# Performance work log

Hardware: AMD Instinct MI355X
Metric: run time of the kernel (lower is better)

The kernel has to match this reference:

```python
import jax, jax.numpy as jnp
import numpy as np

N = 100_000        # nodes
E = 800_000        # directed edges before symmetrization
IN_DIM = 18        # input_dim_wf + input_dim_vm
HID = 128
VM_NUM = 16        # each_vm_type_num * vm_types
B = 65536 // VM_NUM
NEG_SLOPE = 0.2    # PyG GATConv leaky_relu slope


def _gat_conv(h, src, dst, W, a_s, a_d, b, n):
    """PyG GATConv (heads=1, add_self_loops=True, dropout off)."""
    z = h @ W                                     # [n, C]
    loops = jnp.arange(n, dtype=src.dtype)
    s = jnp.concatenate([src, loops])
    d = jnp.concatenate([dst, loops])
    e_s = z @ a_s                                 # [n]
    e_d = z @ a_d
    alpha = jax.nn.leaky_relu(e_s[s] + e_d[d], NEG_SLOPE)   # [E']
    amax = jax.ops.segment_max(alpha, d, num_segments=n)    # stable softmax over incoming edges
    ex = jnp.exp(alpha - amax[d])
    denom = jax.ops.segment_sum(ex, d, num_segments=n)
    w = ex / denom[d]
    out = jax.ops.segment_sum(w[:, None] * z[s], d, num_segments=n)
    return out + b


def setup_inputs() -> dict:
    key = jax.random.key(0)
    ks = jax.random.split(key, 16)
    sc = 0.1
    inp = {
        'state_wf': jax.random.normal(ks[0], (N, IN_DIM), jnp.float32),
        'edge_index': jax.random.randint(ks[1], (2, E), 0, N, jnp.int32),
        'candidate_task_index': jax.random.randint(ks[2], (B * VM_NUM,), 0, N, jnp.int32),
        # GAT layer 0: 18 -> 128
        'W0': jax.random.normal(ks[3], (IN_DIM, HID), jnp.float32) * sc,
        'a_src0': jax.random.normal(ks[4], (HID,), jnp.float32) * sc,
        'a_dst0': jax.random.normal(ks[5], (HID,), jnp.float32) * sc,
        'b0': jnp.zeros((HID,), jnp.float32),
        # GAT layer 1: 128 -> 128
        'W1': jax.random.normal(ks[6], (HID, HID), jnp.float32) * sc,
        'a_src1': jax.random.normal(ks[7], (HID,), jnp.float32) * sc,
        'a_dst1': jax.random.normal(ks[8], (HID,), jnp.float32) * sc,
        'b1': jnp.zeros((HID,), jnp.float32),
        # actor MLP: Linear(128,128) + ReLU + Linear(128,1)
        'mW0': jax.random.normal(ks[9], (HID, HID), jnp.float32) * sc,
        'mb0': jnp.zeros((HID,), jnp.float32),
        'mW1': jax.random.normal(ks[10], (HID, 1), jnp.float32) * sc,
        'mb1': jnp.zeros((1,), jnp.float32),
    }
    return inp


def reference(state_wf, edge_index, candidate_task_index,
              W0, a_src0, a_dst0, b0, W1, a_src1, a_dst1, b1,
              mW0, mb0, mW1, mb1):
    # Actor.forward symmetrizes edges: cat(edge_index, edge_index.flip(0))
    src = jnp.concatenate([edge_index[0], edge_index[1]])
    dst = jnp.concatenate([edge_index[1], edge_index[0]])
    # GAT stack, F.elu after each conv (dropout=0)
    h = jax.nn.elu(_gat_conv(state_wf, src, dst, W0, a_src0, a_dst0, b0, N))
    h = jax.nn.elu(_gat_conv(h, src, dst, W1, a_src1, a_dst1, b1, N))
    # gather candidate tasks and score them
    cand = h[candidate_task_index].reshape(-1, VM_NUM, HID)       # [B, vm, H]
    scores = jax.nn.relu(cand @ mW0 + mb0) @ mW1 + mb1            # [B, vm, 1]
    pi = jax.nn.softmax(scores, axis=1)[..., 0]                   # softmax over dim=1
    return pi
```

## Files before the change

kernel.cpp:

```cpp
#include <hip/hip_runtime.h>
#include <hip/hip_bf16.h>
#include <math.h>
#include <stdint.h>

typedef __hip_bfloat16 bf16;
typedef __attribute__((ext_vector_type(8))) short s8v;
typedef __attribute__((ext_vector_type(4))) float f4v;

#define N_NODES 100000
#define HID 128
#define NEG 0.2f
#define NBUCK 256
#define BSHIFT 9
#define INDIM 18
#define CAP 10240

__device__ __forceinline__ float b2f(bf16 x) { return __bfloat162float(x); }
__device__ __forceinline__ bf16 f2b(float x) { return __float2bfloat16(x); }
__device__ __forceinline__ float lo_bf(unsigned int u) {
    union { unsigned int i; float f; } c; c.i = u << 16; return c.f;
}
__device__ __forceinline__ float hi_bf(unsigned int u) {
    union { unsigned int i; float f; } c; c.i = u & 0xffff0000u; return c.f;
}
__device__ __forceinline__ short bfbits(float x) {
    union { bf16 b; short s; } u; u.b = f2b(x); return u.s;
}


__device__ void pack128(const float* __restrict__ W, short* __restrict__ frag, int b) {
    int idx = b * 256 + threadIdx.x;
    int j = idx & 7;
    int lane = (idx >> 3) & 63;
    int cb = (idx >> 9) & 7;
    int kb = idx >> 12;
    int k = kb * 32 + (lane >> 4) * 8 + j;
    int c = cb * 16 + (lane & 15);
    float w = W[k * HID + c];
    bf16 hi = f2b(w);
    frag[idx] = bfbits(w);
    frag[16384 + idx] = bfbits(w - b2f(hi));
}

__global__ __launch_bounds__(256) void k_prep(const float* __restrict__ W1,
                          const float* __restrict__ mW0, const float* __restrict__ W0,
                          short* __restrict__ W1f, short* __restrict__ mW0f,
                          short* __restrict__ W0f, int* __restrict__ bnext) {
    int b = blockIdx.x;
    int t = threadIdx.x;
    if (b < 64) { pack128(W1, W1f, b); return; }
    if (b < 128) { pack128(mW0, mW0f, b - 64); return; }
    if (b < 192) {
        int idx = (b - 128) * 256 + t;
        int var = idx >> 13;
        int r = idx & 8191;
        int j = r & 7;
        int lane = (r >> 3) & 63;
        int cb = (r >> 9) & 7;
        int kb = r >> 12;
        int kp = kb * 32 + (lane >> 4) * 8 + j;
        int c = cb * 16 + (lane & 15);
        short out = 0;
        if (kp < 2 * INDIM) {
            int src = (kp < INDIM) ? kp : kp - INDIM;
            float w = W0[src * HID + c];
            bf16 hi = f2b(w);
            bool want_hi = (kp < INDIM) ^ (var == 1);
            out = want_hi ? bfbits(w) : bfbits(w - b2f(hi));
        }
        W0f[var * 8192 + r] = out;
        return;
    }
    bnext[t] = t * CAP;
}


#define SCH 2048
#define SK 8
__global__ __launch_bounds__(256) void k_scat_feat0(const int* __restrict__ ei, int E,
                        int* __restrict__ bnext, unsigned* __restrict__ pairs, int nscat,
                        const float* __restrict__ x, const short* __restrict__ Wf,
                        const float* __restrict__ as_, const float* __restrict__ ad_,
                        bf16* __restrict__ z, float* __restrict__ es, float* __restrict__ ed,
                        int n) {
    __shared__ int h[NBUCK], base[NBUCK], h2[NBUCK];
    __shared__ __align__(16) short ztile[4][16][136];
    if (blockIdx.x < (unsigned)nscat) {
        int t = threadIdx.x;
        h[t] = 0; h2[t] = 0;
        __syncthreads();
        int b0 = blockIdx.x * SCH;
        int eu[SK], ev[SK];
#pragma unroll
        for (int k = 0; k < SK; k++) {
            int i = b0 + k * 256 + t;
            if (i < E) {
                int u = ei[i], v = ei[E + i];
                eu[k] = u; ev[k] = v;
                atomicAdd(&h[v >> BSHIFT], 1);
                atomicAdd(&h[u >> BSHIFT], 1);
            } else { eu[k] = -1; ev[k] = -1; }
        }
        __syncthreads();
        if (h[t] > 0) base[t] = atomicAdd(&bnext[t], h[t]);
        __syncthreads();
#pragma unroll
        for (int k = 0; k < SK; k++) {
            if (eu[k] >= 0) {
                unsigned u = (unsigned)eu[k], v = (unsigned)ev[k];
                int bv = v >> BSHIFT;
                pairs[base[bv] + atomicAdd(&h2[bv], 1)] = ((v & 511u) << 17) | u;
                int bu = u >> BSHIFT;
                pairs[base[bu] + atomicAdd(&h2[bu], 1)] = ((u & 511u) << 17) | v;
            }
        }
        return;
    }
    int fb = blockIdx.x - nscat;
    int wv = threadIdx.x >> 6, lane = threadIdx.x & 63;
    int node0 = (fb * 4 + wv) * 16;
    if (node0 >= n) return;
    int m = lane & 15, q = lane >> 4;
    const float* xr = x + (size_t)(node0 + m) * INDIM;
    s8v af0, af1;
#pragma unroll
    for (int j = 0; j < 8; j++) {
        int p0 = q * 8 + j;
        float v0 = 0.f;
        if (p0 < INDIM) v0 = xr[p0];
        else if (p0 < 2 * INDIM) v0 = xr[p0 - INDIM];
        short o0;
        if (p0 < INDIM) o0 = bfbits(v0);
        else o0 = bfbits(v0 - b2f(f2b(v0)));
        af0[j] = o0;
        int p1 = 32 + q * 8 + j;
        float v1 = (p1 < 2 * INDIM) ? xr[p1 - INDIM] : 0.f;
        af1[j] = bfbits(v1 - b2f(f2b(v1)));
    }
    f4v acc[8];
#pragma unroll
    for (int cb = 0; cb < 8; cb++) acc[cb] = (f4v){0.f, 0.f, 0.f, 0.f};
    const s8v* wf = (const s8v*)Wf;
#pragma unroll
    for (int cb = 0; cb < 8; cb++) {
        acc[cb] = __builtin_amdgcn_mfma_f32_16x16x32_bf16(af0, wf[cb * 64 + lane], acc[cb], 0, 0, 0);
        acc[cb] = __builtin_amdgcn_mfma_f32_16x16x32_bf16(af1, wf[(8 + cb) * 64 + lane], acc[cb], 0, 0, 0);
        acc[cb] = __builtin_amdgcn_mfma_f32_16x16x32_bf16(af0, wf[1024 + cb * 64 + lane], acc[cb], 0, 0, 0);
        acc[cb] = __builtin_amdgcn_mfma_f32_16x16x32_bf16(af1, wf[1024 + (8 + cb) * 64 + lane], acc[cb], 0, 0, 0);
    }
    float pe[4] = {0.f, 0.f, 0.f, 0.f}, pd[4] = {0.f, 0.f, 0.f, 0.f};
#pragma unroll
    for (int cb = 0; cb < 8; cb++) {
        float asv = as_[cb * 16 + m];
        float adv = ad_[cb * 16 + m];
#pragma unroll
        for (int r = 0; r < 4; r++) { pe[r] += acc[cb][r] * asv; pd[r] += acc[cb][r] * adv; }
    }
#pragma unroll
    for (int r = 0; r < 4; r++) {
#pragma unroll
        for (int off = 1; off < 16; off <<= 1) {
            pe[r] += __shfl_xor(pe[r], off);
            pd[r] += __shfl_xor(pd[r], off);
        }
    }
    if (m == 0) {
#pragma unroll
        for (int r = 0; r < 4; r++) {
            es[node0 + q * 4 + r] = pe[r];
            ed[node0 + q * 4 + r] = pd[r];
        }
    }
#pragma unroll
    for (int cb = 0; cb < 8; cb++)
#pragma unroll
        for (int r = 0; r < 4; r++)
            ztile[wv][q * 4 + r][cb * 16 + m] = bfbits(acc[cb][r]);
#pragma unroll
    for (int i = 0; i < 4; i++) {
        int idx = i * 64 + lane;
        int row = idx >> 4, t = idx & 15;
        s8v v = *(const s8v*)&ztile[wv][row][t * 8];
        *(s8v*)((short*)z + (size_t)(node0 + row) * HID + t * 8) = v;
    }
}


__global__ __launch_bounds__(256) void k_bbuild(const unsigned* __restrict__ pairs,
                                                const int* __restrict__ bnext,
                                                int* __restrict__ rowptr,
                                                int* __restrict__ col, int n) {
    __shared__ int deg[512];
    __shared__ int off[512];
    __shared__ int s2[2][256];
    __shared__ int exs[256];
    int t = threadIdx.x;
    int b = blockIdx.x;
    int node0 = b << BSHIFT;
    int cnt = bnext[t] - t * CAP;
    s2[0][t] = cnt;
    __syncthreads();
    int cur = 0;
    for (int o = 1; o < 256; o <<= 1) {
        int x2 = s2[cur][t] + ((t >= o) ? s2[cur][t - o] : 0);
        s2[cur ^ 1][t] = x2;
        cur ^= 1;
        __syncthreads();
    }
    exs[t] = s2[cur][t] - cnt;
    __syncthreads();
    int out0 = exs[b];
    int in0 = b * CAP;
    int cnt_b = bnext[b] - in0;
    deg[t] = 0; deg[t + 256] = 0;
    __syncthreads();
    for (int i = t; i < cnt_b; i += 256) atomicAdd(&deg[pairs[in0 + i] >> 17], 1);
    __syncthreads();
    int a0 = deg[2 * t], a1 = deg[2 * t + 1];
    int s = a0 + a1;
    s2[0][t] = s;
    __syncthreads();
    cur = 0;
    for (int o = 1; o < 256; o <<= 1) {
        int x2 = s2[cur][t] + ((t >= o) ? s2[cur][t - o] : 0);
        s2[cur ^ 1][t] = x2;
        cur ^= 1;
        __syncthreads();
    }
    int excl = s2[cur][t] - s;
    off[2 * t] = excl;
    off[2 * t + 1] = excl + a0;
    __syncthreads();
    for (int j = t; j < 512; j += 256) {
        int node = node0 + j;
        if (node <= n) rowptr[node] = out0 + off[j];
    }
    deg[t] = 0; deg[t + 256] = 0;
    __syncthreads();
    for (int i = t; i < cnt_b; i += 256) {
        unsigned pr = pairs[in0 + i];
        int d = pr >> 17;
        int ofs = atomicAdd(&deg[d], 1);
        col[out0 + off[d] + ofs] = (int)(pr & 0x1FFFFu);
    }
}


__global__ __launch_bounds__(256) void k_aggfeat1(const bf16* __restrict__ z,
                      const int* __restrict__ rowptr, const int* __restrict__ col,
                      const float* __restrict__ es, const float* __restrict__ ed,
                      const float* __restrict__ bias,
                      const short* __restrict__ Wf, const float* __restrict__ as1,
                      const float* __restrict__ ad1,
                      bf16* __restrict__ zout, float* __restrict__ es1,
                      float* __restrict__ ed1, int n) {
    __shared__ __align__(16) short htile[16][136];
    __shared__ __align__(16) short ztile[16][136];
    __shared__ float red[4][16][2];
    int wv = threadIdx.x >> 6, lane = threadIdx.x & 63;
    int node0 = blockIdx.x * 16;
    int g = lane >> 4, t = lane & 15;
    const uint4* zr = (const uint4*)z;
    for (int i = 0; i < 4; i++) {
        int d = node0 + wv * 4 + i;
        int s0 = rowptr[d], s1 = rowptr[d + 1];
        float edv = ed[d];
        float acc[8];
#pragma unroll
        for (int j = 0; j < 8; j++) acc[j] = 0.f;
        float den = 0.f;
        for (int e0 = s0; e0 < s1; e0 += 8) {
            int eA = e0 + g, eB = e0 + 4 + g;
            bool okA = (eA < s1), okB = (eB < s1);
            int sA = col[okA ? eA : s1 - 1];
            int sB = col[okB ? eB : s1 - 1];
            float aA = es[sA] + edv; aA = aA > 0.f ? aA : NEG * aA;
            float aB = es[sB] + edv; aB = aB > 0.f ? aB : NEG * aB;
            float pA = okA ? __expf(fminf(aA, 15.f)) : 0.f;
            float pB = okB ? __expf(fminf(aB, 15.f)) : 0.f;
            uint4 rA = zr[(size_t)sA * 16 + t];
            uint4 rB = zr[(size_t)sB * 16 + t];
            den += pA + pB;
            acc[0] += pA * lo_bf(rA.x) + pB * lo_bf(rB.x);
            acc[1] += pA * hi_bf(rA.x) + pB * hi_bf(rB.x);
            acc[2] += pA * lo_bf(rA.y) + pB * lo_bf(rB.y);
            acc[3] += pA * hi_bf(rA.y) + pB * hi_bf(rB.y);
            acc[4] += pA * lo_bf(rA.z) + pB * lo_bf(rB.z);
            acc[5] += pA * hi_bf(rA.z) + pB * hi_bf(rB.z);
            acc[6] += pA * lo_bf(rA.w) + pB * lo_bf(rB.w);
            acc[7] += pA * hi_bf(rA.w) + pB * hi_bf(rB.w);
        }
#pragma unroll
        for (int off = 16; off <= 32; off <<= 1) {
            den += __shfl_xor(den, off);
#pragma unroll
            for (int j = 0; j < 8; j++) acc[j] += __shfl_xor(acc[j], off);
        }
        if (g == 0) {
            float aself = es[d] + edv;
            aself = aself > 0.f ? aself : NEG * aself;
            float pself = __expf(fminf(aself, 15.f));
            den += pself;
            uint4 raw = zr[(size_t)d * 16 + t];
            acc[0] += pself * lo_bf(raw.x); acc[1] += pself * hi_bf(raw.x);
            acc[2] += pself * lo_bf(raw.y); acc[3] += pself * hi_bf(raw.y);
            acc[4] += pself * lo_bf(raw.z); acc[5] += pself * hi_bf(raw.z);
            acc[6] += pself * lo_bf(raw.w); acc[7] += pself * hi_bf(raw.w);
            float inv = 1.f / den;
            union { bf16 hv[8]; uint4 v; } uo;
#pragma unroll
            for (int j = 0; j < 8; j++) {
                float o = acc[j] * inv + bias[t * 8 + j];
                o = o > 0.f ? o : (__expf(o) - 1.f);
                uo.hv[j] = f2b(o);
            }
            *((uint4*)&htile[wv * 4 + i][t * 8]) = uo.v;
        }
    }
    __syncthreads();
    int m = lane & 15, q = lane >> 4;
    s8v af[4];
#pragma unroll
    for (int kb = 0; kb < 4; kb++) af[kb] = *(const s8v*)&htile[m][kb * 32 + q * 8];
    f4v fac[2];
    fac[0] = (f4v){0.f, 0.f, 0.f, 0.f};
    fac[1] = (f4v){0.f, 0.f, 0.f, 0.f};
    const s8v* wf = (const s8v*)Wf;
#pragma unroll
    for (int kb = 0; kb < 4; kb++) {
#pragma unroll
        for (int c = 0; c < 2; c++) {
            int cb = 2 * wv + c;
            fac[c] = __builtin_amdgcn_mfma_f32_16x16x32_bf16(af[kb], wf[(kb * 8 + cb) * 64 + lane], fac[c], 0, 0, 0);
            fac[c] = __builtin_amdgcn_mfma_f32_16x16x32_bf16(af[kb], wf[2048 + (kb * 8 + cb) * 64 + lane], fac[c], 0, 0, 0);
        }
    }
    float pe[4] = {0.f, 0.f, 0.f, 0.f}, pd[4] = {0.f, 0.f, 0.f, 0.f};
#pragma unroll
    for (int c = 0; c < 2; c++) {
        int cb = 2 * wv + c;
        float asv = as1[cb * 16 + m];
        float adv = ad1[cb * 16 + m];
#pragma unroll
        for (int r = 0; r < 4; r++) { pe[r] += fac[c][r] * asv; pd[r] += fac[c][r] * adv; }
    }
#pragma unroll
    for (int r = 0; r < 4; r++) {
#pragma unroll
        for (int off = 1; off < 16; off <<= 1) {
            pe[r] += __shfl_xor(pe[r], off);
            pd[r] += __shfl_xor(pd[r], off);
        }
    }
    if (m == 0) {
#pragma unroll
        for (int r = 0; r < 4; r++) {
            red[wv][q * 4 + r][0] = pe[r];
            red[wv][q * 4 + r][1] = pd[r];
        }
    }
#pragma unroll
    for (int c = 0; c < 2; c++) {
        int cb = 2 * wv + c;
#pragma unroll
        for (int r = 0; r < 4; r++)
            ztile[q * 4 + r][cb * 16 + m] = bfbits(fac[c][r]);
    }
    __syncthreads();
    int tid = threadIdx.x;
    if (tid < 16) es1[node0 + tid] = red[0][tid][0] + red[1][tid][0] + red[2][tid][0] + red[3][tid][0];
    else if (tid < 32) {
        int c = tid - 16;
        ed1[node0 + c] = red[0][c][1] + red[1][c][1] + red[2][c][1] + red[3][c][1];
    }
    int row = tid >> 4, tt = tid & 15;
    s8v v = *(const s8v*)&ztile[row][tt * 8];
    *(s8v*)((short*)zout + (size_t)(node0 + row) * HID + tt * 8) = v;
}


__global__ __launch_bounds__(256) void k_agg(const bf16* __restrict__ z,
                      const int* __restrict__ rowptr, const int* __restrict__ col,
                      const float* __restrict__ es, const float* __restrict__ ed,
                      const float* __restrict__ bias, bf16* __restrict__ hout, int n) {
    int wv = threadIdx.x >> 6;
    int lane = threadIdx.x & 63;
    int d = blockIdx.x * 4 + wv;
    if (d >= n) return;
    int s0 = rowptr[d], s1 = rowptr[d + 1];
    float edv = ed[d];
    int g = lane >> 4, t = lane & 15;
    const uint4* zr = (const uint4*)z;
    float acc[8];
#pragma unroll
    for (int j = 0; j < 8; j++) acc[j] = 0.f;
    float den = 0.f;
    for (int e0 = s0; e0 < s1; e0 += 8) {
        int eA = e0 + g, eB = e0 + 4 + g;
        bool okA = (eA < s1), okB = (eB < s1);
        int sA = col[okA ? eA : s1 - 1];
        int sB = col[okB ? eB : s1 - 1];
        float aA = es[sA] + edv; aA = aA > 0.f ? aA : NEG * aA;
        float aB = es[sB] + edv; aB = aB > 0.f ? aB : NEG * aB;
        float pA = okA ? __expf(fminf(aA, 15.f)) : 0.f;
        float pB = okB ? __expf(fminf(aB, 15.f)) : 0.f;
        uint4 rA = zr[(size_t)sA * 16 + t];
        uint4 rB = zr[(size_t)sB * 16 + t];
        den += pA + pB;
        acc[0] += pA * lo_bf(rA.x) + pB * lo_bf(rB.x);
        acc[1] += pA * hi_bf(rA.x) + pB * hi_bf(rB.x);
        acc[2] += pA * lo_bf(rA.y) + pB * lo_bf(rB.y);
        acc[3] += pA * hi_bf(rA.y) + pB * hi_bf(rB.y);
        acc[4] += pA * lo_bf(rA.z) + pB * lo_bf(rB.z);
        acc[5] += pA * hi_bf(rA.z) + pB * hi_bf(rB.z);
        acc[6] += pA * lo_bf(rA.w) + pB * lo_bf(rB.w);
        acc[7] += pA * hi_bf(rA.w) + pB * hi_bf(rB.w);
    }
#pragma unroll
    for (int off = 16; off <= 32; off <<= 1) {
        den += __shfl_xor(den, off);
#pragma unroll
        for (int j = 0; j < 8; j++) acc[j] += __shfl_xor(acc[j], off);
    }
    if (g == 0) {
        float aself = es[d] + edv;
        aself = aself > 0.f ? aself : NEG * aself;
        float pself = __expf(fminf(aself, 15.f));
        den += pself;
        uint4 raw = zr[(size_t)d * 16 + t];
        acc[0] += pself * lo_bf(raw.x); acc[1] += pself * hi_bf(raw.x);
        acc[2] += pself * lo_bf(raw.y); acc[3] += pself * hi_bf(raw.y);
        acc[4] += pself * lo_bf(raw.z); acc[5] += pself * hi_bf(raw.z);
        acc[6] += pself * lo_bf(raw.w); acc[7] += pself * hi_bf(raw.w);
        float inv = 1.f / den;
        union { bf16 hv[8]; uint4 v; } uo;
#pragma unroll
        for (int j = 0; j < 8; j++) {
            float o = acc[j] * inv + bias[t * 8 + j];
            o = o > 0.f ? o : (__expf(o) - 1.f);
            uo.hv[j] = f2b(o);
        }
        ((uint4*)hout)[(size_t)d * 16 + t] = uo.v;
    }
}


__global__ __launch_bounds__(256) void k_group(const bf16* __restrict__ h,
                        const int* __restrict__ cand,
                        const short* __restrict__ Wf, const float* __restrict__ mb0,
                        const float* __restrict__ mW1, const float* __restrict__ mb1,
                        float* __restrict__ out) {
    __shared__ float sc[4][16];
    int wv = threadIdx.x >> 6, lane = threadIdx.x & 63;
    int g = blockIdx.x * 4 + wv;
    int m = lane & 15, q = lane >> 4;
    int node = cand[g * 16 + m];
    const short* hrow = (const short*)h + (size_t)node * HID + q * 8;
    s8v af[4];
#pragma unroll
    for (int kb = 0; kb < 4; kb++) af[kb] = *(const s8v*)(hrow + kb * 32);
    f4v acc[8];
#pragma unroll
    for (int cb = 0; cb < 8; cb++) acc[cb] = (f4v){0.f, 0.f, 0.f, 0.f};
    const s8v* wf = (const s8v*)Wf;
#pragma unroll
    for (int kb = 0; kb < 4; kb++) {
#pragma unroll
        for (int cb = 0; cb < 8; cb++) {
            acc[cb] = __builtin_amdgcn_mfma_f32_16x16x32_bf16(af[kb], wf[(kb * 8 + cb) * 64 + lane], acc[cb], 0, 0, 0);
            acc[cb] = __builtin_amdgcn_mfma_f32_16x16x32_bf16(af[kb], wf[2048 + (kb * 8 + cb) * 64 + lane], acc[cb], 0, 0, 0);
        }
    }
    float sr[4] = {0.f, 0.f, 0.f, 0.f};
#pragma unroll
    for (int cb = 0; cb < 8; cb++) {
        float b0v = mb0[cb * 16 + m];
        float w1v = mW1[cb * 16 + m];
#pragma unroll
        for (int r = 0; r < 4; r++) sr[r] += fmaxf(acc[cb][r] + b0v, 0.f) * w1v;
    }
#pragma unroll
    for (int r = 0; r < 4; r++) {
#pragma unroll
        for (int off = 1; off < 16; off <<= 1) sr[r] += __shfl_xor(sr[r], off);
    }
    float b1v = mb1[0];
    if (m == 0) {
#pragma unroll
        for (int r = 0; r < 4; r++) sc[wv][q * 4 + r] = sr[r] + b1v;
    }
    if (lane < 16) {
        float s = sc[wv][lane];
        float mx = s;
#pragma unroll
        for (int off = 1; off < 16; off <<= 1) mx = fmaxf(mx, __shfl_xor(mx, off));
        float e = __expf(s - mx);
        float den = e;
#pragma unroll
        for (int off = 1; off < 16; off <<= 1) den += __shfl_xor(den, off);
        out[g * 16 + lane] = e / den;
    }
}


extern "C" void kernel_launch(void* const* d_in, const int* in_sizes, int n_in,
                              void* d_out, int out_size, void* d_ws, size_t ws_size,
                              hipStream_t stream) {
    const int N = N_NODES;
    const float* state = (const float*)d_in[0];
    const int* ei   = (const int*)d_in[1];
    const int* cand = (const int*)d_in[2];
    const float* W0  = (const float*)d_in[3];
    const float* as0 = (const float*)d_in[4];
    const float* ad0 = (const float*)d_in[5];
    const float* b0  = (const float*)d_in[6];
    const float* W1  = (const float*)d_in[7];
    const float* as1 = (const float*)d_in[8];
    const float* ad1 = (const float*)d_in[9];
    const float* b1  = (const float*)d_in[10];
    const float* mW0 = (const float*)d_in[11];
    const float* mb0 = (const float*)d_in[12];
    const float* mW1 = (const float*)d_in[13];
    const float* mb1 = (const float*)d_in[14];

    int E = in_sizes[1] / 2;
    int M = 2 * E;
    int ncand = in_sizes[2];
    int ngroups = ncand / 16;

    char* p = (char*)d_ws;
    bf16* zb = (bf16*)p;              p += (size_t)N * HID * 2;
    bf16* hb = (bf16*)p;              p += (size_t)N * HID * 2;
    float* es = (float*)p;            p += (size_t)N * 4;
    float* ed = (float*)p;            p += (size_t)N * 4;
    float* es1 = (float*)p;           p += (size_t)N * 4;
    float* ed1 = (float*)p;           p += (size_t)N * 4;
    p = (char*)(((uintptr_t)p + 15) & ~(uintptr_t)15);
    short* W1frag  = (short*)p;       p += 32768 * 2;
    short* mW0frag = (short*)p;       p += 32768 * 2;
    short* W0frag  = (short*)p;       p += 16384 * 2;
    int* rowptr = (int*)p;            p += (size_t)(N + 1) * 4;
    int* col    = (int*)p;            p += (size_t)M * 4;
    unsigned* pairs = (unsigned*)p;   p += (size_t)NBUCK * CAP * 4;
    int* bnext  = (int*)p;            p += NBUCK * 4;

    int nwb = N / 4;
    int nfb = (N / 16 + 3) / 4;
    int nscat = (E + SCH - 1) / SCH;

    k_prep<<<193, 256, 0, stream>>>(W1, mW0, W0, W1frag, mW0frag, W0frag, bnext);
    k_scat_feat0<<<nscat + nfb, 256, 0, stream>>>(ei, E, bnext, pairs, nscat,
                                                  state, W0frag, as0, ad0, zb, es, ed, N);
    k_bbuild<<<NBUCK, 256, 0, stream>>>(pairs, bnext, rowptr, col, N);
    k_aggfeat1<<<N / 16, 256, 0, stream>>>(zb, rowptr, col, es, ed, b0,
                                           W1frag, as1, ad1, hb, es1, ed1, N);
    k_agg<<<nwb, 256, 0, stream>>>(hb, rowptr, col, es1, ed1, b1, zb, N);
    k_group<<<ngroups / 4, 256, 0, stream>>>(zb, cand, mW0frag, mb0, mW1, mb1, (float*)d_out);
}
```

Baseline: 310.7 us.

## Make each wave own 16 nodes in fused layer-1 aggregate+transform, drop block barriers

Restructures k_aggfeat1 so each wavefront aggregates 16 destination nodes and then computes the full 128-column projection for its own tile, instead of four waves sharing a 16-node tile and splitting the columns. This removes both __syncthreads barriers and the cross-wave shared-memory reduction of the attention logits, so waves with short neighbour lists no longer wait on slow ones. In exchange each wave holds 8 MFMA accumulators (more registers, possibly lower occupancy), loads the whole W1 fragment set per wave, and the grid has a quarter as many blocks.

```diff
diff --git a/kernel.cpp b/kernel.cpp
--- a/kernel.cpp
+++ b/kernel.cpp
@@ -254,15 +254,14 @@
                       const float* __restrict__ ad1,
                       bf16* __restrict__ zout, float* __restrict__ es1,
                       float* __restrict__ ed1, int n) {
-    __shared__ __align__(16) short htile[16][136];
-    __shared__ __align__(16) short ztile[16][136];
-    __shared__ float red[4][16][2];
+    __shared__ __align__(16) short htile[4][16][136];
     int wv = threadIdx.x >> 6, lane = threadIdx.x & 63;
-    int node0 = blockIdx.x * 16;
+    int node0 = blockIdx.x * 64 + wv * 16;
+    if (node0 >= n) return;
     int g = lane >> 4, t = lane & 15;
     const uint4* zr = (const uint4*)z;
-    for (int i = 0; i < 4; i++) {
-        int d = node0 + wv * 4 + i;
+    for (int i = 0; i < 16; i++) {
+        int d = node0 + i;
         int s0 = rowptr[d], s1 = rowptr[d + 1];
         float edv = ed[d];
         float acc[8];
@@ -314,35 +313,32 @@
                 o = o > 0.f ? o : (__expf(o) - 1.f);
                 uo.hv[j] = f2b(o);
             }
-            *((uint4*)&htile[wv * 4 + i][t * 8]) = uo.v;
-        }
-    }
-    __syncthreads();
+            *((uint4*)&htile[wv][i][t * 8]) = uo.v;
+        }
+    }
     int m = lane & 15, q = lane >> 4;
     s8v af[4];
 #pragma unroll
-    for (int kb = 0; kb < 4; kb++) af[kb] = *(const s8v*)&htile[m][kb * 32 + q * 8];
-    f4v fac[2];
-    fac[0] = (f4v){0.f, 0.f, 0.f, 0.f};
-    fac[1] = (f4v){0.f, 0.f, 0.f, 0.f};
+    for (int kb = 0; kb < 4; kb++) af[kb] = *(const s8v*)&htile[wv][m][kb * 32 + q * 8];
+    f4v fac[8];
+#pragma unroll
+    for (int cb = 0; cb < 8; cb++) fac[cb] = (f4v){0.f, 0.f, 0.f, 0.f};
     const s8v* wf = (const s8v*)Wf;
 #pragma unroll
     for (int kb = 0; kb < 4; kb++) {
 #pragma unroll
-        for (int c = 0; c < 2; c++) {
-            int cb = 2 * wv + c;
-            fac[c] = __builtin_amdgcn_mfma_f32_16x16x32_bf16(af[kb], wf[(kb * 8 + cb) * 64 + lane], fac[c], 0, 0, 0);
-            fac[c] = __builtin_amdgcn_mfma_f32_16x16x32_bf16(af[kb], wf[2048 + (kb * 8 + cb) * 64 + lane], fac[c], 0, 0, 0);
+        for (int cb = 0; cb < 8; cb++) {
+            fac[cb] = __builtin_amdgcn_mfma_f32_16x16x32_bf16(af[kb], wf[(kb * 8 + cb) * 64 + lane], fac[cb], 0, 0, 0);
+            fac[cb] = __builtin_amdgcn_mfma_f32_16x16x32_bf16(af[kb], wf[2048 + (kb * 8 + cb) * 64 + lane], fac[cb], 0, 0, 0);
         }
     }
     float pe[4] = {0.f, 0.f, 0.f, 0.f}, pd[4] = {0.f, 0.f, 0.f, 0.f};
 #pragma unroll
-    for (int c = 0; c < 2; c++) {
-        int cb = 2 * wv + c;
+    for (int cb = 0; cb < 8; cb++) {
         float asv = as1[cb * 16 + m];
         float adv = ad1[cb * 16 + m];
 #pragma unroll
-        for (int r = 0; r < 4; r++) { pe[r] += fac[c][r] * asv; pd[r] += fac[c][r] * adv; }
+        for (int r = 0; r < 4; r++) { pe[r] += fac[cb][r] * asv; pd[r] += fac[cb][r] * adv; }
     }
 #pragma unroll
     for (int r = 0; r < 4; r++) {
@@ -355,27 +351,22 @@
     if (m == 0) {
 #pragma unroll
         for (int r = 0; r < 4; r++) {
-            red[wv][q * 4 + r][0] = pe[r];
-            red[wv][q * 4 + r][1] = pd[r];
-        }
-    }
-#pragma unroll
-    for (int c = 0; c < 2; c++) {
-        int cb = 2 * wv + c;
+            es1[node0 + q * 4 + r] = pe[r];
+            ed1[node0 + q * 4 + r] = pd[r];
+        }
+    }
+#pragma unroll
+    for (int cb = 0; cb < 8; cb++)
 #pragma unroll
         for (int r = 0; r < 4; r++)
-            ztile[q * 4 + r][cb * 16 + m] = bfbits(fac[c][r]);
-    }
-    __syncthreads();
-    int tid = threadIdx.x;
-    if (tid < 16) es1[node0 + tid] = red[0][tid][0] + red[1][tid][0] + red[2][tid][0] + red[3][tid][0];
-    else if (tid < 32) {
-        int c = tid - 16;
-        ed1[node0 + c] = red[0][c][1] + red[1][c][1] + red[2][c][1] + red[3][c][1];
-    }
-    int row = tid >> 4, tt = tid & 15;
-    s8v v = *(const s8v*)&ztile[row][tt * 8];
-    *(s8v*)((short*)zout + (size_t)(node0 + row) * HID + tt * 8) = v;
+            htile[wv][q * 4 + r][cb * 16 + m] = bfbits(fac[cb][r]);
+#pragma unroll
+    for (int i = 0; i < 4; i++) {
+        int idx = i * 64 + lane;
+        int row = idx >> 4, tt = idx & 15;
+        s8v v = *(const s8v*)&htile[wv][row][tt * 8];
+        *(s8v*)((short*)zout + (size_t)(node0 + row) * HID + tt * 8) = v;
+    }
 }
 
 
@@ -547,13 +538,14 @@
     int nwb = N / 4;
     int nfb = (N / 16 + 3) / 4;
     int nscat = (E + SCH - 1) / SCH;
+    int nafb = (N + 63) / 64;
 
     k_prep<<<193, 256, 0, stream>>>(W1, mW0, W0, W1frag, mW0frag, W0frag, bnext);
     k_scat_feat0<<<nscat + nfb, 256, 0, stream>>>(ei, E, bnext, pairs, nscat,
                                                   state, W0frag, as0, ad0, zb, es, ed, N);
     k_bbuild<<<NBUCK, 256, 0, stream>>>(pairs, bnext, rowptr, col, N);
-    k_aggfeat1<<<N / 16, 256, 0, stream>>>(zb, rowptr, col, es, ed, b0,
-                                           W1frag, as1, ad1, hb, es1, ed1, N);
+    k_aggfeat1<<<nafb, 256, 0, stream>>>(zb, rowptr, col, es, ed, b0,
+                                         W1frag, as1, ad1, hb, es1, ed1, N);
     k_agg<<<nwb, 256, 0, stream>>>(hb, rowptr, col, es1, ed1, b1, zb, N);
     k_group<<<ngroups / 4, 256, 0, stream>>>(zb, cand, mW0frag, mb0, mW1, mb1, (float*)d_out);
 }
```

New measurement: 350.9 us. 1.13x slower.
